# Optimization experiments

Measured on AMD Instinct MI355X. Metric: run time of the kernel, lower is better.

## Reference

```python
import jax, jax.numpy as jnp
import numpy as np

N_ENTITY = 30000
N_REL = 12
N_BASES = 8
KG_DIM = 128
TOK_DIM = 768
B = 32
N_CTX_ENT = 50
SEQ = 256
N_EDGES = 400000
VOCAB = 30522
PAD_IDX = 0


def setup_inputs() -> dict:
    key = jax.random.key(0)
    ks = jax.random.split(key, 24)
    s = 0.02
    inp = {
        "context_entities": jax.random.randint(ks[0], (B, N_CTX_ENT), 0, N_ENTITY),
        "context_tokens": jax.random.randint(ks[1], (B, SEQ), 0, VOCAB),
        "edge_index": jax.random.randint(ks[2], (2, N_EDGES), 0, N_ENTITY),
        "edge_type": jax.random.randint(ks[3], (N_EDGES,), 0, N_REL),
        # stand-in for bert_model(...).last_hidden_state
        "token_embedding": jax.random.normal(ks[4], (B, SEQ, TOK_DIM), dtype=jnp.float32),
        # RGCN basis-decomposition params (x=None -> node-identity features)
        "comp": jax.random.normal(ks[5], (N_REL, N_BASES), dtype=jnp.float32) * s,
        "basis": jax.random.normal(ks[6], (N_BASES, N_ENTITY, KG_DIM), dtype=jnp.float32) * s,
        "root": jax.random.normal(ks[7], (N_ENTITY, KG_DIM), dtype=jnp.float32) * s,
        "rgcn_bias": jnp.zeros((KG_DIM,), dtype=jnp.float32),
        # SelfDotAttention over entity reps (dim=da=KG_DIM)
        "ent_W": jax.random.normal(ks[8], (KG_DIM, KG_DIM), dtype=jnp.float32) * s,
        "ent_b": jnp.zeros((KG_DIM,), dtype=jnp.float32),
        "ent_v": jax.random.normal(ks[9], (KG_DIM,), dtype=jnp.float32) * s,
        # AdditiveAttention over token reps (dim=da=TOK_DIM)
        "tok_W": jax.random.normal(ks[10], (TOK_DIM, TOK_DIM), dtype=jnp.float32) * s,
        "tok_b": jnp.zeros((TOK_DIM,), dtype=jnp.float32),
        "tok_v": jax.random.normal(ks[11], (TOK_DIM,), dtype=jnp.float32) * s,
        # linear_transformation: token_emb_dim -> kg_emb_dim
        "lin_W": jax.random.normal(ks[12], (KG_DIM, TOK_DIM), dtype=jnp.float32) * s,
        "lin_b": jnp.zeros((KG_DIM,), dtype=jnp.float32),
        # gating: 2*kg_emb_dim -> kg_emb_dim
        "gate_W": jax.random.normal(ks[13], (KG_DIM, 2 * KG_DIM), dtype=jnp.float32) * s,
        "gate_b": jnp.zeros((KG_DIM,), dtype=jnp.float32),
    }
    return inp


def _rgcn(comp, basis, root, bias, edge_index, edge_type):
    # composed per-relation weight over identity features: [R, N, D]
    weight = jnp.einsum('rb,bnd->rnd', comp, basis)
    src, dst = edge_index[0], edge_index[1]
    msg = weight[edge_type, src]                      # [E, D] gather
    # per-relation, per-target mean aggregation (PyG RGCNConv aggr='mean')
    seg = edge_type * N_ENTITY + dst
    cnt = jax.ops.segment_sum(jnp.ones((msg.shape[0],), msg.dtype), seg,
                              num_segments=N_REL * N_ENTITY)
    norm = 1.0 / jnp.maximum(cnt[seg], 1.0)
    agg = jax.ops.segment_sum(msg * norm[:, None], dst, num_segments=N_ENTITY)
    return agg + root + bias                          # [N, D]


def _attn_pool(h, mask, W, b, v):
    # e = v^T tanh(h W + b); masked softmax; weighted sum over sequence
    e = jnp.einsum('bld,d->bl', jnp.tanh(jnp.einsum('bld,de->ble', h, W) + b), v)
    e = jnp.where(mask, e, jnp.asarray(-1e9, h.dtype))
    a = jax.nn.softmax(e, axis=-1)
    return jnp.einsum('bl,bld->bd', a, h)


def reference(context_entities, context_tokens, edge_index, edge_type,
              token_embedding, comp, basis, root, rgcn_bias,
              ent_W, ent_b, ent_v, tok_W, tok_b, tok_v,
              lin_W, lin_b, gate_W, gate_b):
    kg_embedding = _rgcn(comp, basis, root, rgcn_bias, edge_index, edge_type)

    entity_reps = kg_embedding[context_entities]              # [B, L_e, D]
    entity_mask = context_entities != PAD_IDX
    entity_attn_rep = _attn_pool(entity_reps, entity_mask, ent_W, ent_b, ent_v)

    token_mask = context_tokens != PAD_IDX
    token_attn_rep = _attn_pool(token_embedding, token_mask, tok_W, tok_b, tok_v)
    token_attn_rep = token_attn_rep @ lin_W.T + lin_b         # [B, D]

    gate = jax.nn.sigmoid(
        jnp.concatenate([token_attn_rep, entity_attn_rep], axis=1) @ gate_W.T + gate_b)
    user_embedding = gate * token_attn_rep + (1.0 - gate) * entity_attn_rep

    scores = user_embedding @ kg_embedding.T                  # [B, N_ENTITY]
    return scores
```

## Files before the change

### kernel.cpp

```cpp
#include <hip/hip_runtime.h>
#include <hip/hip_bf16.h>
#include <math.h>

#define N_ENTITY 30000
#define N_REL    12
#define N_BASES  8
#define KG_DIM   128
#define TOK_DIM  768
#define BATCH    32
#define N_CTX    50
#define SEQ      256
#define N_EDGES  400000

#define W8_SCALE 1024.0f
#define W8_INV   (1.0f / 1024.0f)

#define OFF_KG     0
#define OFF_CNT    3840000
#define OFF_DEG    4200000
#define OFF_START  4230000
#define OFF_CURSOR 4260004
#define OFF_CHUNK  4290004
#define OFF_SR     4290068
#define OFF_ETOK   5090068
#define OFF_ENT    5098260
#define OFF_TOK    5102356
#define OFF_USER   5106452
#define OFF_W      5110548
#define OFF_ABF    5110548
#define OFF_WBF    8256276
#define NEED_W_BYTES ((size_t)(OFF_W + 11520000) * 4)

typedef __bf16 bf16x8 __attribute__((ext_vector_type(8)));
typedef float  floatx4 __attribute__((ext_vector_type(4)));

__device__ __forceinline__ float tanh_fast(float x) {
    float ax = fabsf(x);
    float e = __expf(-2.0f * ax);
    float t = 1.0f - 2.0f * e / (1.0f + e);
    return copysignf(t, x);
}

__global__ void zero_kernel(int* __restrict__ p, int n) {
    int i = blockIdx.x * 256 + threadIdx.x;
    if (i < n) p[i] = 0;
}

__global__ void count_kernel(const int* __restrict__ edge_index,
                             const int* __restrict__ edge_type,
                             int* __restrict__ cnt) {
    int e = blockIdx.x * 256 + threadIdx.x;
    if (e >= N_EDGES) return;
    int r = edge_type[e];
    int dst = edge_index[N_EDGES + e];
    atomicAdd(&cnt[r * N_ENTITY + dst], 1);
}

__global__ __launch_bounds__(1024) void scan1_kernel(const int* __restrict__ cnt,
                                                     int* __restrict__ deg,
                                                     int* __restrict__ start,
                                                     int* __restrict__ chunksum) {
    __shared__ int wsum[16];
    int tid = threadIdx.x, lane = tid & 63, wv = tid >> 6;
    int i = blockIdx.x * 1024 + tid;
    int v = 0;
    if (i < N_ENTITY) {
#pragma unroll
        for (int r = 0; r < N_REL; ++r) v += cnt[r * N_ENTITY + i];
        deg[i] = v;
    }
    int x = v;
#pragma unroll
    for (int off = 1; off < 64; off <<= 1) {
        int t = __shfl_up(x, off);
        if (lane >= off) x += t;
    }
    if (lane == 63) wsum[wv] = x;
    __syncthreads();
    if (wv == 0 && lane < 16) {
        int w = wsum[lane];
#pragma unroll
        for (int off = 1; off < 16; off <<= 1) {
            int t = __shfl_up(w, off);
            if (lane >= off) w += t;
        }
        wsum[lane] = w;
    }
    __syncthreads();
    int wbase = (wv == 0) ? 0 : wsum[wv - 1];
    if (i < N_ENTITY) start[i] = wbase + x - v;
    if (tid == 1023) chunksum[blockIdx.x] = wbase + x;
}

__global__ __launch_bounds__(256) void scan2_kernel(const int* __restrict__ chunksum,
                                                    int* __restrict__ chunkoff,
                                                    int* __restrict__ start,
                                                    int* __restrict__ zp) {
    int tid = threadIdx.x;
    if (tid < 64) {
        int lane = tid;
        int v = (lane < 30) ? chunksum[lane] : 0;
        int x = v;
#pragma unroll
        for (int off = 1; off < 64; off <<= 1) {
            int t = __shfl_up(x, off);
            if (lane >= off) x += t;
        }
        if (lane < 30) chunkoff[lane] = x - v;
        if (lane == 63) start[N_ENTITY] = x;
    }
    for (int i = tid; i < 20480; i += 256) zp[i] = 0;
}

__global__ __launch_bounds__(1024) void scan3_kernel(const int* __restrict__ chunkoff,
                                                     int* __restrict__ start,
                                                     int* __restrict__ cursor) {
    int i = blockIdx.x * 1024 + threadIdx.x;
    if (i < N_ENTITY) {
        int s = start[i] + chunkoff[blockIdx.x];
        start[i] = s;
        cursor[i] = s;
    }
}

__global__ void place_kernel(const int* __restrict__ edge_index,
                             const int* __restrict__ edge_type,
                             const int* __restrict__ cnt,
                             int* __restrict__ cursor,
                             int2* __restrict__ er) {
    int e = blockIdx.x * 256 + threadIdx.x;
    if (e >= N_EDGES) return;
    int r = edge_type[e];
    int src = edge_index[e];
    int dst = edge_index[N_EDGES + e];
    int c = cnt[r * N_ENTITY + dst];
    float norm = 1.0f / (float)(c > 1 ? c : 1);
    int slot = atomicAdd(&cursor[dst], 1);
    er[slot] = make_int2(src | (r << 15), __float_as_int(norm));
}

__global__ void weight_fp8_kernel(const float* __restrict__ comp,
                                  const float4* __restrict__ basis4,
                                  unsigned int* __restrict__ w1) {
    int idx = blockIdx.x * 256 + threadIdx.x;
    float4 bv[N_BASES];
#pragma unroll
    for (int i = 0; i < N_BASES; ++i) bv[i] = basis4[(size_t)i * 960000 + idx];
#pragma unroll
    for (int r = 0; r < N_REL; ++r) {
        float s0 = 0.f, s1 = 0.f, s2 = 0.f, s3 = 0.f;
#pragma unroll
        for (int i = 0; i < N_BASES; ++i) {
            float c = comp[r * N_BASES + i];
            s0 += c * bv[i].x; s1 += c * bv[i].y;
            s2 += c * bv[i].z; s3 += c * bv[i].w;
        }
        int pk = __builtin_amdgcn_cvt_pk_fp8_f32(s0 * W8_SCALE, s1 * W8_SCALE, 0, false);
        pk = __builtin_amdgcn_cvt_pk_fp8_f32(s2 * W8_SCALE, s3 * W8_SCALE, pk, true);
        w1[(size_t)r * 960000 + idx] = (unsigned int)pk;
    }
}

__global__ __launch_bounds__(256) void gather_kernel(const int* __restrict__ start,
                                                     const int* __restrict__ deg,
                                                     const int2* __restrict__ er,
                                                     const unsigned short* __restrict__ w8,
                                                     const float2* __restrict__ root2,
                                                     const float2* __restrict__ bias2,
                                                     float2* __restrict__ kg2) {
    int wv = threadIdx.x >> 6, lane = threadIdx.x & 63;
    int dst = blockIdx.x * 4 + wv;
    if (dst >= N_ENTITY) return;
    int s = start[dst], n = deg[dst];
    float ax = 0.f, ay = 0.f;
    int j = 0;
    for (; j + 1 < n; j += 2) {
        int2 e0 = er[s + j], e1 = er[s + j + 1];
        float n0 = __int_as_float(e0.y), n1 = __int_as_float(e1.y);
        int s0 = e0.x & 32767, r0 = e0.x >> 15;
        int s1 = e1.x & 32767, r1 = e1.x >> 15;
        int u0 = (int)w8[((size_t)(r0 * N_ENTITY + s0) << 6) + lane];
        int u1 = (int)w8[((size_t)(r1 * N_ENTITY + s1) << 6) + lane];
        ax += __builtin_amdgcn_cvt_f32_fp8(u0, 0) * n0 +
              __builtin_amdgcn_cvt_f32_fp8(u1, 0) * n1;
        ay += __builtin_amdgcn_cvt_f32_fp8(u0, 1) * n0 +
              __builtin_amdgcn_cvt_f32_fp8(u1, 1) * n1;
    }
    if (j < n) {
        int2 e0 = er[s + j];
        float n0 = __int_as_float(e0.y);
        int s0 = e0.x & 32767, r0 = e0.x >> 15;
        int u0 = (int)w8[((size_t)(r0 * N_ENTITY + s0) << 6) + lane];
        ax += __builtin_amdgcn_cvt_f32_fp8(u0, 0) * n0;
        ay += __builtin_amdgcn_cvt_f32_fp8(u0, 1) * n0;
    }
    float2 rt = root2[(size_t)dst * 64 + lane];
    float2 bs = bias2[lane];
    kg2[(size_t)dst * 64 + lane] = make_float2(ax * W8_INV + rt.x + bs.x,
                                               ay * W8_INV + rt.y + bs.y);
}

__global__ __launch_bounds__(256) void gather_otf_kernel(const int* __restrict__ start,
                                                         const int* __restrict__ deg,
                                                         const int2* __restrict__ er,
                                                         const float* __restrict__ comp,
                                                         const float2* __restrict__ basis2,
                                                         const float2* __restrict__ root2,
                                                         const float2* __restrict__ bias2,
                                                         float2* __restrict__ kg2) {
    int wv = threadIdx.x >> 6, lane = threadIdx.x & 63;
    int dst = blockIdx.x * 4 + wv;
    if (dst >= N_ENTITY) return;
    int s = start[dst], n = deg[dst];
    float ax = 0.f, ay = 0.f;
    for (int j = 0; j < n; ++j) {
        int2 e0 = er[s + j];
        float nm = __int_as_float(e0.y);
        int src = e0.x & 32767, r = e0.x >> 15;
        float mx = 0.f, my = 0.f;
#pragma unroll
        for (int b = 0; b < N_BASES; ++b) {
            float cf = comp[r * N_BASES + b];
            float2 bs = basis2[((size_t)b * N_ENTITY + src) * 64 + lane];
            mx += cf * bs.x; my += cf * bs.y;
        }
        ax += mx * nm; ay += my * nm;
    }
    float2 rt = root2[(size_t)dst * 64 + lane];
    float2 bs = bias2[lane];
    kg2[(size_t)dst * 64 + lane] = make_float2(ax + rt.x + bs.x, ay + rt.y + bs.y);
}

__global__ __launch_bounds__(256) void ent_attn_kernel(const int* __restrict__ ctx_ent,
                                                       const float* __restrict__ kg,
                                                       const float* __restrict__ W,
                                                       const float* __restrict__ bb,
                                                       const float* __restrict__ v,
                                                       float* __restrict__ ent_rep) {
    __shared__ __align__(16) float Ws[KG_DIM * KG_DIM];
    __shared__ __align__(16) float h[N_CTX * KG_DIM];
    __shared__ float es[64];
    __shared__ int ids[N_CTX];
    int b = blockIdx.x, tid = threadIdx.x;
    if (tid < N_CTX) ids[tid] = ctx_ent[b * N_CTX + tid];
    __syncthreads();
    for (int i = tid; i < N_CTX * 32; i += 256) {
        int l = i >> 5, d4 = i & 31;
        ((float4*)h)[i] = ((const float4*)kg)[(size_t)ids[l] * 32 + d4];
    }
    for (int i = tid; i < KG_DIM * KG_DIM / 4; i += 256)
        ((float4*)Ws)[i] = ((const float4*)W)[i];
    __syncthreads();

    int wave = tid >> 6, lane = tid & 63;
    const int nl = (N_CTX - wave + 3) / 4;
    float s0[13], s1[13];
#pragma unroll
    for (int i = 0; i < 13; ++i) { s0[i] = 0.f; s1[i] = 0.f; }
    for (int k4 = 0; k4 < 32; ++k4) {
        float4 hk[13];
#pragma unroll
        for (int i = 0; i < 13; ++i)
            if (i < nl) hk[i] = ((const float4*)h)[(wave + i * 4) * 32 + k4];
#pragma unroll
        for (int kk = 0; kk < 4; ++kk) {
            int k = k4 * 4 + kk;
            float w0 = Ws[k * KG_DIM + lane];
            float w1 = Ws[k * KG_DIM + lane + 64];
#pragma unroll
            for (int i = 0; i < 13; ++i) {
                if (i < nl) {
                    float hv = (&hk[i].x)[kk];
                    s0[i] += hv * w0;
                    s1[i] += hv * w1;
                }
            }
        }
    }
    float bias0 = bb[lane], bias1 = bb[lane + 64];
    float v0 = v[lane], v1 = v[lane + 64];
    for (int i = 0; i < nl; ++i) {
        int l = wave + i * 4;
        float p = tanhf(s0[i] + bias0) * v0 + tanhf(s1[i] + bias1) * v1;
        p += __shfl_xor(p, 32); p += __shfl_xor(p, 16); p += __shfl_xor(p, 8);
        p += __shfl_xor(p, 4);  p += __shfl_xor(p, 2);  p += __shfl_xor(p, 1);
        if (lane == 0) es[l] = p;
    }
    __syncthreads();
    if (tid < 64) {
        float val = (tid < N_CTX && ids[tid] != 0) ? es[tid] : -1e9f;
        float mx = val;
        mx = fmaxf(mx, __shfl_xor(mx, 32)); mx = fmaxf(mx, __shfl_xor(mx, 16));
        mx = fmaxf(mx, __shfl_xor(mx, 8));  mx = fmaxf(mx, __shfl_xor(mx, 4));
        mx = fmaxf(mx, __shfl_xor(mx, 2));  mx = fmaxf(mx, __shfl_xor(mx, 1));
        float ex = (tid < N_CTX) ? expf(val - mx) : 0.f;
        float sm = ex;
        sm += __shfl_xor(sm, 32); sm += __shfl_xor(sm, 16); sm += __shfl_xor(sm, 8);
        sm += __shfl_xor(sm, 4);  sm += __shfl_xor(sm, 2);  sm += __shfl_xor(sm, 1);
        if (tid < N_CTX) es[tid] = ex / sm;
    }
    __syncthreads();
    if (tid < KG_DIM) {
        float o = 0.f;
#pragma unroll
        for (int l = 0; l < N_CTX; ++l) o += es[l] * h[l * KG_DIM + tid];
        ent_rep[b * KG_DIM + tid] = o;
    }
}


__global__ void convA_kernel(const float* __restrict__ in, __bf16* __restrict__ out,
                             int n8) {
    int i = blockIdx.x * 256 + threadIdx.x;
    if (i >= n8) return;
    const float4* p = (const float4*)(in + (size_t)i * 8);
    float4 a = p[0], b = p[1];
    union { __bf16 h[8]; uint4 u; } r;
    r.h[0] = (__bf16)a.x; r.h[1] = (__bf16)a.y; r.h[2] = (__bf16)a.z; r.h[3] = (__bf16)a.w;
    r.h[4] = (__bf16)b.x; r.h[5] = (__bf16)b.y; r.h[6] = (__bf16)b.z; r.h[7] = (__bf16)b.w;
    *(uint4*)(out + (size_t)i * 8) = r.u;
}

__global__ void convWT_kernel(const float* __restrict__ W, __bf16* __restrict__ Wt) {
    __shared__ float tile[64][65];
    int tx = threadIdx.x & 63, ty = threadIdx.x >> 6;
    int kb = blockIdx.x * 64, cb = blockIdx.y * 64;
#pragma unroll
    for (int i = 0; i < 16; ++i) {
        int r = ty + i * 4;
        tile[r][tx] = W[(size_t)(kb + r) * TOK_DIM + cb + tx];
    }
    __syncthreads();
#pragma unroll
    for (int i = 0; i < 16; ++i) {
        int r = ty + i * 4;
        Wt[(size_t)(cb + r) * TOK_DIM + kb + tx] = (__bf16)tile[tx][r];
    }
}

__global__ __launch_bounds__(256) void tok_gemm_kernel(const __bf16* __restrict__ A,
                                                       const __bf16* __restrict__ Bt,
                                                       const float* __restrict__ bias,
                                                       const float* __restrict__ v,
                                                       float* __restrict__ e_out) {
    __shared__ __align__(16) __bf16 sA[4096];
    __shared__ __align__(16) __bf16 sB[4096];
    int tid = threadIdx.x;
    int wave = tid >> 6, lane = tid & 63;
    int wm = wave >> 1, wn = wave & 1;
    int quad = lane >> 4, idx = lane & 15;
    int m0 = blockIdx.y * 128, c0 = blockIdx.x * 128;

    int rowS = tid & 127, kpS = tid >> 7;
    const __bf16* gA0 = A + (size_t)(m0 + rowS) * TOK_DIM + kpS * 8;
    const __bf16* gA1 = gA0 + 16;
    const __bf16* gB0 = Bt + (size_t)(c0 + rowS) * TOK_DIM + kpS * 8;
    const __bf16* gB1 = gB0 + 16;
    __bf16* dA0 = &sA[tid * 8];
    __bf16* dA1 = &sA[tid * 8 + 2048];
    __bf16* dB0 = &sB[tid * 8];
    __bf16* dB1 = &sB[tid * 8 + 2048];

    floatx4 acc[4][4];
#pragma unroll
    for (int mi = 0; mi < 4; ++mi)
#pragma unroll
        for (int ni = 0; ni < 4; ++ni)
            acc[mi][ni] = (floatx4){0.f, 0.f, 0.f, 0.f};

    for (int k0 = 0; k0 < TOK_DIM; k0 += 32) {
        uint4 ra0 = *(const uint4*)(gA0 + k0);
        uint4 ra1 = *(const uint4*)(gA1 + k0);
        uint4 rb0 = *(const uint4*)(gB0 + k0);
        uint4 rb1 = *(const uint4*)(gB1 + k0);
        __syncthreads();
        *(uint4*)dA0 = ra0; *(uint4*)dA1 = ra1;
        *(uint4*)dB0 = rb0; *(uint4*)dB1 = rb1;
        __syncthreads();
        bf16x8 aF[4], bF[4];
#pragma unroll
        for (int i = 0; i < 4; ++i) {
            aF[i] = *(const bf16x8*)&sA[quad * 1024 + (wm * 64 + i * 16 + idx) * 8];
            bF[i] = *(const bf16x8*)&sB[quad * 1024 + (wn * 64 + i * 16 + idx) * 8];
        }
#pragma unroll
        for (int mi = 0; mi < 4; ++mi)
#pragma unroll
            for (int ni = 0; ni < 4; ++ni)
                acc[mi][ni] = __builtin_amdgcn_mfma_f32_16x16x32_bf16(
                    aF[mi], bF[ni], acc[mi][ni], 0, 0, 0);
    }

    float bv[4], vv[4];
#pragma unroll
    for (int ni = 0; ni < 4; ++ni) {
        int c = c0 + wn * 64 + ni * 16 + idx;
        bv[ni] = bias[c]; vv[ni] = v[c];
    }
#pragma unroll
    for (int mi = 0; mi < 4; ++mi) {
        float s[4] = {0.f, 0.f, 0.f, 0.f};
#pragma unroll
        for (int ni = 0; ni < 4; ++ni)
#pragma unroll
            for (int r = 0; r < 4; ++r)
                s[r] += tanh_fast(acc[mi][ni][r] + bv[ni]) * vv[ni];
#pragma unroll
        for (int r = 0; r < 4; ++r) {
            s[r] += __shfl_xor(s[r], 1); s[r] += __shfl_xor(s[r], 2);
            s[r] += __shfl_xor(s[r], 4); s[r] += __shfl_xor(s[r], 8);
        }
        if (idx == 0) {
            int rbase = m0 + wm * 64 + mi * 16 + quad * 4;
#pragma unroll
            for (int r = 0; r < 4; ++r) atomicAdd(&e_out[rbase + r], s[r]);
        }
    }
}

__global__ __launch_bounds__(256) void tok_pool2_kernel(const int* __restrict__ ctx_tok,
                                                        const float* __restrict__ e_ws,
                                                        const __bf16* __restrict__ Abf,
                                                        const float* __restrict__ lin_W,
                                                        float* __restrict__ tok_rep) {
    __shared__ float a_s[SEQ];
    __shared__ float4 part[8][32];
    __shared__ __align__(16) float pooled[128];
    __shared__ float redm[4];
    __shared__ float reds[4];
    int b = blockIdx.x, c = blockIdx.y;
    int tid = threadIdx.x;
    int wave = tid >> 6, lane = tid & 63;
    int t = ctx_tok[b * SEQ + tid];
    float val = (t != 0) ? e_ws[b * SEQ + tid] : -1e9f;
    float mx = val;
    mx = fmaxf(mx, __shfl_xor(mx, 32)); mx = fmaxf(mx, __shfl_xor(mx, 16));
    mx = fmaxf(mx, __shfl_xor(mx, 8));  mx = fmaxf(mx, __shfl_xor(mx, 4));
    mx = fmaxf(mx, __shfl_xor(mx, 2));  mx = fmaxf(mx, __shfl_xor(mx, 1));
    if (lane == 0) redm[wave] = mx;
    __syncthreads();
    mx = fmaxf(fmaxf(redm[0], redm[1]), fmaxf(redm[2], redm[3]));
    float ex = expf(val - mx);
    float sm = ex;
    sm += __shfl_xor(sm, 32); sm += __shfl_xor(sm, 16); sm += __shfl_xor(sm, 8);
    sm += __shfl_xor(sm, 4);  sm += __shfl_xor(sm, 2);  sm += __shfl_xor(sm, 1);
    if (lane == 0) reds[wave] = sm;
    __syncthreads();
    sm = reds[0] + reds[1] + reds[2] + reds[3];
    a_s[tid] = ex / sm;
    __syncthreads();
    int d4 = tid & 31, lg = tid >> 5;
    const unsigned int* eb = (const unsigned int*)(Abf + (size_t)b * SEQ * TOK_DIM +
                                                   c * 128 + d4 * 4);
    float4 acc = make_float4(0.f, 0.f, 0.f, 0.f);
    for (int l = lg; l < SEQ; l += 8) {
        float al = a_s[l];
        unsigned int u0 = eb[(size_t)l * 384];
        unsigned int u1 = eb[(size_t)l * 384 + 1];
        acc.x += al * __uint_as_float(u0 << 16);
        acc.y += al * __uint_as_float(u0 & 0xffff0000u);
        acc.z += al * __uint_as_float(u1 << 16);
        acc.w += al * __uint_as_float(u1 & 0xffff0000u);
    }
    part[lg][d4] = acc;
    __syncthreads();
    if (tid < 32) {
        float4 s = part[0][tid];
#pragma unroll
        for (int g = 1; g < 8; ++g) {
            float4 p = part[g][tid];
            s.x += p.x; s.y += p.y; s.z += p.z; s.w += p.w;
        }
        ((float4*)pooled)[tid] = s;
    }
    __syncthreads();
    int d = tid & 127, hf = tid >> 7;
    const float* wr = lin_W + (size_t)d * TOK_DIM + c * 128 + hf * 64;
    float s = 0.f;
#pragma unroll 8
    for (int k = 0; k < 64; ++k) s += pooled[hf * 64 + k] * wr[k];
    atomicAdd(&tok_rep[b * KG_DIM + d], s);
}

__global__ void gate_kernel(const float* __restrict__ tok_rep,
                            const float* __restrict__ lin_b,
                            const float* __restrict__ ent_rep,
                            const float* __restrict__ gate_W,
                            const float* __restrict__ gate_b,
                            float* __restrict__ user) {
    __shared__ float tr[KG_DIM], er[KG_DIM];
    int b = blockIdx.x, d = threadIdx.x;
    tr[d] = tok_rep[b * KG_DIM + d] + lin_b[d];
    er[d] = ent_rep[b * KG_DIM + d];
    __syncthreads();
    float g = gate_b[d];
    const float* wr = gate_W + (size_t)d * 256;
#pragma unroll 8
    for (int k = 0; k < KG_DIM; ++k) g += tr[k] * wr[k] + er[k] * wr[KG_DIM + k];
    float sig = 1.f / (1.f + expf(-g));
    user[b * KG_DIM + d] = sig * tr[d] + (1.f - sig) * er[d];
}

__global__ void scores_kernel(const float* __restrict__ user,
                              const float4* __restrict__ kg4,
                              float* __restrict__ out) {
    __shared__ float4 u4[BATCH * 32];
    int tid = threadIdx.x;
    for (int i = tid; i < BATCH * 32; i += 256) u4[i] = ((const float4*)user)[i];
    __syncthreads();
    int n = blockIdx.x * 256 + tid;
    if (n >= N_ENTITY) return;
    float acc[BATCH];
#pragma unroll
    for (int b = 0; b < BATCH; ++b) acc[b] = 0.f;
    for (int d4 = 0; d4 < 32; ++d4) {
        float4 k = kg4[(size_t)n * 32 + d4];
#pragma unroll
        for (int b = 0; b < BATCH; ++b) {
            float4 u = u4[b * 32 + d4];
            acc[b] += k.x * u.x + k.y * u.y + k.z * u.z + k.w * u.w;
        }
    }
    for (int b = 0; b < BATCH; ++b) out[(size_t)b * N_ENTITY + n] = acc[b];
}

extern "C" void kernel_launch(void* const* d_in, const int* in_sizes, int n_in,
                              void* d_out, int out_size, void* d_ws, size_t ws_size,
                              hipStream_t stream) {
    (void)in_sizes; (void)n_in; (void)out_size;
    const int*   ctx_ent   = (const int*)d_in[0];
    const int*   ctx_tok   = (const int*)d_in[1];
    const int*   edge_index= (const int*)d_in[2];
    const int*   edge_type = (const int*)d_in[3];
    const float* tok_emb   = (const float*)d_in[4];
    const float* comp      = (const float*)d_in[5];
    const float* basis     = (const float*)d_in[6];
    const float* root      = (const float*)d_in[7];
    const float* rgcn_bias = (const float*)d_in[8];
    const float* ent_W     = (const float*)d_in[9];
    const float* ent_b     = (const float*)d_in[10];
    const float* ent_v     = (const float*)d_in[11];
    const float* tok_W     = (const float*)d_in[12];
    const float* tok_b     = (const float*)d_in[13];
    const float* tok_v     = (const float*)d_in[14];
    const float* lin_W     = (const float*)d_in[15];
    const float* lin_b     = (const float*)d_in[16];
    const float* gate_W    = (const float*)d_in[17];
    const float* gate_b    = (const float*)d_in[18];
    float* scores = (float*)d_out;

    float* ws = (float*)d_ws;
    float* kg      = ws + OFF_KG;
    int*   cnt     = (int*)(ws + OFF_CNT);
    int*   deg     = (int*)(ws + OFF_DEG);
    int*   start   = (int*)(ws + OFF_START);
    int*   cursor  = (int*)(ws + OFF_CURSOR);
    int*   chunk   = (int*)(ws + OFF_CHUNK);
    int2*  er      = (int2*)(ws + OFF_SR);
    float* e_ws    = ws + OFF_ETOK;
    float* ent_rep = ws + OFF_ENT;
    float* tok_rep = ws + OFF_TOK;
    float* user    = ws + OFF_USER;
    float* weight  = ws + OFF_W;
    __bf16* Abf    = (__bf16*)(ws + OFF_ABF);
    __bf16* Wbf    = (__bf16*)(ws + OFF_WBF);
    const bool use_weight = (ws_size >= NEED_W_BYTES);

    zero_kernel<<<(360000 + 255) / 256, 256, 0, stream>>>(cnt, 360000);
    count_kernel<<<(N_EDGES + 255) / 256, 256, 0, stream>>>(edge_index, edge_type, cnt);
    scan1_kernel<<<30, 1024, 0, stream>>>(cnt, deg, start, chunk);
    scan2_kernel<<<1, 256, 0, stream>>>(chunk, chunk + 32, start, (int*)e_ws);
    scan3_kernel<<<30, 1024, 0, stream>>>(chunk + 32, start, cursor);
    place_kernel<<<(N_EDGES + 255) / 256, 256, 0, stream>>>(edge_index, edge_type, cnt,
                                                            cursor, er);
    if (use_weight) {
        weight_fp8_kernel<<<3750, 256, 0, stream>>>(comp, (const float4*)basis,
                                                    (unsigned int*)weight);
        gather_kernel<<<(N_ENTITY + 3) / 4, 256, 0, stream>>>(
            start, deg, er, (const unsigned short*)weight, (const float2*)root,
            (const float2*)rgcn_bias, (float2*)kg);
    } else {
        gather_otf_kernel<<<(N_ENTITY + 3) / 4, 256, 0, stream>>>(
            start, deg, er, comp, (const float2*)basis, (const float2*)root,
            (const float2*)rgcn_bias, (float2*)kg);
    }
    ent_attn_kernel<<<BATCH, 256, 0, stream>>>(ctx_ent, kg, ent_W, ent_b, ent_v, ent_rep);

    convA_kernel<<<(BATCH * SEQ * TOK_DIM / 8 + 255) / 256, 256, 0, stream>>>(
        tok_emb, Abf, BATCH * SEQ * TOK_DIM / 8);
    {
        dim3 g(12, 12);
        convWT_kernel<<<g, 256, 0, stream>>>(tok_W, Wbf);
    }
    {
        dim3 g(TOK_DIM / 128, BATCH * SEQ / 128);
        tok_gemm_kernel<<<g, 256, 0, stream>>>(Abf, Wbf, tok_b, tok_v, e_ws);
    }
    {
        dim3 g(BATCH, 6);
        tok_pool2_kernel<<<g, 256, 0, stream>>>(ctx_tok, e_ws, Abf, lin_W, tok_rep);
    }
    gate_kernel<<<BATCH, 128, 0, stream>>>(tok_rep, lin_b, ent_rep, gate_W, gate_b, user);
    scores_kernel<<<(N_ENTITY + 255) / 256, 256, 0, stream>>>(user, (const float4*)kg, scores);
}
```

Baseline: 470.2 us.

## Fuse independent kernels into combined launches to cut launch count and overlap work

```diff
diff --git a/kernel.cpp b/kernel.cpp
--- a/kernel.cpp
+++ b/kernel.cpp
@@ -15,21 +15,29 @@
 #define W8_SCALE 1024.0f
 #define W8_INV   (1.0f / 1024.0f)
 
+#define NCHUNK 118
+
 #define OFF_KG     0
 #define OFF_CNT    3840000
 #define OFF_DEG    4200000
 #define OFF_START  4230000
-#define OFF_CURSOR 4260004
-#define OFF_CHUNK  4290004
-#define OFF_SR     4290068
-#define OFF_ETOK   5090068
-#define OFF_ENT    5098260
-#define OFF_TOK    5102356
-#define OFF_USER   5106452
-#define OFF_W      5110548
-#define OFF_ABF    5110548
-#define OFF_WBF    8256276
-#define NEED_W_BYTES ((size_t)(OFF_W + 11520000) * 4)
+#define OFF_PC     4260000
+#define OFF_CHK    4290000
+#define OFF_SR     4290256
+#define OFF_ETOK   5090256
+#define OFF_ENT    5098448
+#define OFF_TOK    5102544
+#define OFF_USER   5106640
+#define OFF_W      5110736
+#define OFF_ABF_B  16630736
+#define OFF_WBF_B  19776464
+#define END_BIG    20071376
+#define NEED_BIG_BYTES ((size_t)END_BIG * 4)
+#define OFF_ABF_S  5110736
+#define OFF_WBF_S  8256464
+
+#define NZERO_INT  410736
+#define NZB        1605
 
 typedef __bf16 bf16x8 __attribute__((ext_vector_type(8)));
 typedef float  floatx4 __attribute__((ext_vector_type(4)));
@@ -41,93 +49,283 @@
     return copysignf(t, x);
 }
 
-__global__ void zero_kernel(int* __restrict__ p, int n) {
-    int i = blockIdx.x * 256 + threadIdx.x;
-    if (i < n) p[i] = 0;
-}
-
-__global__ void count_kernel(const int* __restrict__ edge_index,
-                             const int* __restrict__ edge_type,
-                             int* __restrict__ cnt) {
-    int e = blockIdx.x * 256 + threadIdx.x;
-    if (e >= N_EDGES) return;
-    int r = edge_type[e];
-    int dst = edge_index[N_EDGES + e];
-    atomicAdd(&cnt[r * N_ENTITY + dst], 1);
-}
-
-__global__ __launch_bounds__(1024) void scan1_kernel(const int* __restrict__ cnt,
-                                                     int* __restrict__ deg,
-                                                     int* __restrict__ start,
-                                                     int* __restrict__ chunksum) {
-    __shared__ int wsum[16];
-    int tid = threadIdx.x, lane = tid & 63, wv = tid >> 6;
-    int i = blockIdx.x * 1024 + tid;
-    int v = 0;
-    if (i < N_ENTITY) {
-#pragma unroll
-        for (int r = 0; r < N_REL; ++r) v += cnt[r * N_ENTITY + i];
-        deg[i] = v;
-    }
-    int x = v;
-#pragma unroll
-    for (int off = 1; off < 64; off <<= 1) {
-        int t = __shfl_up(x, off);
-        if (lane >= off) x += t;
-    }
-    if (lane == 63) wsum[wv] = x;
-    __syncthreads();
-    if (wv == 0 && lane < 16) {
-        int w = wsum[lane];
-#pragma unroll
-        for (int off = 1; off < 16; off <<= 1) {
-            int t = __shfl_up(w, off);
-            if (lane >= off) w += t;
-        }
-        wsum[lane] = w;
-    }
-    __syncthreads();
-    int wbase = (wv == 0) ? 0 : wsum[wv - 1];
-    if (i < N_ENTITY) start[i] = wbase + x - v;
-    if (tid == 1023) chunksum[blockIdx.x] = wbase + x;
-}
-
-__global__ __launch_bounds__(256) void scan2_kernel(const int* __restrict__ chunksum,
-                                                    int* __restrict__ chunkoff,
-                                                    int* __restrict__ start,
-                                                    int* __restrict__ zp) {
-    int tid = threadIdx.x;
-    if (tid < 64) {
-        int lane = tid;
-        int v = (lane < 30) ? chunksum[lane] : 0;
-        int x = v;
+__global__ __launch_bounds__(256) void init_fused_kernel(
+    const float* __restrict__ comp, const float4* __restrict__ basis4,
+    unsigned int* __restrict__ w1,
+    const float* __restrict__ tok_emb, __bf16* __restrict__ Abf,
+    const float* __restrict__ tok_W, __bf16* __restrict__ Wbf,
+    int* __restrict__ cnt, int* __restrict__ pc, int* __restrict__ chk,
+    int* __restrict__ accum, int wB) {
+    __shared__ float tile[64][65];
+    int bid = blockIdx.x, tid = threadIdx.x;
+    if (bid < wB) {
+        int idx = bid * 256 + tid;
+        float4 bv[N_BASES];
+#pragma unroll
+        for (int i = 0; i < N_BASES; ++i) bv[i] = basis4[(size_t)i * 960000 + idx];
+#pragma unroll
+        for (int r = 0; r < N_REL; ++r) {
+            float s0 = 0.f, s1 = 0.f, s2 = 0.f, s3 = 0.f;
+#pragma unroll
+            for (int i = 0; i < N_BASES; ++i) {
+                float c = comp[r * N_BASES + i];
+                s0 += c * bv[i].x; s1 += c * bv[i].y;
+                s2 += c * bv[i].z; s3 += c * bv[i].w;
+            }
+            int pk = __builtin_amdgcn_cvt_pk_fp8_f32(s0 * W8_SCALE, s1 * W8_SCALE, 0, false);
+            pk = __builtin_amdgcn_cvt_pk_fp8_f32(s2 * W8_SCALE, s3 * W8_SCALE, pk, true);
+            w1[(size_t)r * 960000 + idx] = (unsigned int)pk;
+        }
+        return;
+    }
+    bid -= wB;
+    if (bid < 3072) {
+        int i = bid * 256 + tid;
+        const float4* p = (const float4*)(tok_emb + (size_t)i * 8);
+        float4 a = p[0], b = p[1];
+        union { __bf16 h[8]; uint4 u; } r;
+        r.h[0] = (__bf16)a.x; r.h[1] = (__bf16)a.y; r.h[2] = (__bf16)a.z; r.h[3] = (__bf16)a.w;
+        r.h[4] = (__bf16)b.x; r.h[5] = (__bf16)b.y; r.h[6] = (__bf16)b.z; r.h[7] = (__bf16)b.w;
+        *(uint4*)(Abf + (size_t)i * 8) = r.u;
+        return;
+    }
+    bid -= 3072;
+    if (bid < NZB) {
+        int idx = bid * 256 + tid;
+        if (idx < 360000) { cnt[idx] = 0; return; }
+        idx -= 360000;
+        if (idx < 30000) { pc[idx] = 0; return; }
+        idx -= 30000;
+        if (idx < 256) { chk[idx] = 0; return; }
+        idx -= 256;
+        if (idx < 20480) accum[idx] = 0;
+        return;
+    }
+    bid -= NZB;
+    int tx = tid & 63, ty = tid >> 6;
+    int kb = (bid % 12) * 64, cb = (bid / 12) * 64;
+#pragma unroll
+    for (int i = 0; i < 16; ++i) {
+        int rr = ty + i * 4;
+        tile[rr][tx] = tok_W[(size_t)(kb + rr) * TOK_DIM + cb + tx];
+    }
+    __syncthreads();
+#pragma unroll
+    for (int i = 0; i < 16; ++i) {
+        int rr = ty + i * 4;
+        Wbf[(size_t)(cb + rr) * TOK_DIM + kb + tx] = (__bf16)tile[tx][rr];
+    }
+}
+
+__global__ __launch_bounds__(256) void count_gemm_kernel(
+    const int* __restrict__ edge_index, const int* __restrict__ edge_type,
+    int* __restrict__ cnt,
+    const __bf16* __restrict__ A, const __bf16* __restrict__ Bt,
+    const float* __restrict__ bias, const float* __restrict__ v,
+    float* __restrict__ e_out) {
+    __shared__ __align__(16) __bf16 sA[4096];
+    __shared__ __align__(16) __bf16 sB[4096];
+    int bid = blockIdx.x, tid = threadIdx.x;
+    if (bid >= 384) {
+        int e = (bid - 384) * 256 + tid;
+        if (e < N_EDGES) {
+            int r = edge_type[e];
+            int dst = edge_index[N_EDGES + e];
+            atomicAdd(&cnt[r * N_ENTITY + dst], 1);
+        }
+        return;
+    }
+    int wave = tid >> 6, lane = tid & 63;
+    int wm = wave >> 1, wn = wave & 1;
+    int quad = lane >> 4, idx = lane & 15;
+    int m0 = (bid / 6) * 128, c0 = (bid % 6) * 128;
+
+    int rowS = tid & 127, kpS = tid >> 7;
+    const __bf16* gA0 = A + (size_t)(m0 + rowS) * TOK_DIM + kpS * 8;
+    const __bf16* gA1 = gA0 + 16;
+    const __bf16* gB0 = Bt + (size_t)(c0 + rowS) * TOK_DIM + kpS * 8;
+    const __bf16* gB1 = gB0 + 16;
+    __bf16* dA0 = &sA[tid * 8];
+    __bf16* dA1 = &sA[tid * 8 + 2048];
+    __bf16* dB0 = &sB[tid * 8];
+    __bf16* dB1 = &sB[tid * 8 + 2048];
+
+    floatx4 acc[4][4];
+#pragma unroll
+    for (int mi = 0; mi < 4; ++mi)
+#pragma unroll
+        for (int ni = 0; ni < 4; ++ni)
+            acc[mi][ni] = (floatx4){0.f, 0.f, 0.f, 0.f};
+
+    for (int k0 = 0; k0 < TOK_DIM; k0 += 32) {
+        uint4 ra0 = *(const uint4*)(gA0 + k0);
+        uint4 ra1 = *(const uint4*)(gA1 + k0);
+        uint4 rb0 = *(const uint4*)(gB0 + k0);
+        uint4 rb1 = *(const uint4*)(gB1 + k0);
+        __syncthreads();
+        *(uint4*)dA0 = ra0; *(uint4*)dA1 = ra1;
+        *(uint4*)dB0 = rb0; *(uint4*)dB1 = rb1;
+        __syncthreads();
+        bf16x8 aF[4], bF[4];
+#pragma unroll
+        for (int i = 0; i < 4; ++i) {
+            aF[i] = *(const bf16x8*)&sA[quad * 1024 + (wm * 64 + i * 16 + idx) * 8];
+            bF[i] = *(const bf16x8*)&sB[quad * 1024 + (wn * 64 + i * 16 + idx) * 8];
+        }
+#pragma unroll
+        for (int mi = 0; mi < 4; ++mi)
+#pragma unroll
+            for (int ni = 0; ni < 4; ++ni)
+                acc[mi][ni] = __builtin_amdgcn_mfma_f32_16x16x32_bf16(
+                    aF[mi], bF[ni], acc[mi][ni], 0, 0, 0);
+    }
+
+    float bv[4], vv[4];
+#pragma unroll
+    for (int ni = 0; ni < 4; ++ni) {
+        int c = c0 + wn * 64 + ni * 16 + idx;
+        bv[ni] = bias[c]; vv[ni] = v[c];
+    }
+#pragma unroll
+    for (int mi = 0; mi < 4; ++mi) {
+        float s[4] = {0.f, 0.f, 0.f, 0.f};
+#pragma unroll
+        for (int ni = 0; ni < 4; ++ni)
+#pragma unroll
+            for (int r = 0; r < 4; ++r)
+                s[r] += tanh_fast(acc[mi][ni][r] + bv[ni]) * vv[ni];
+#pragma unroll
+        for (int r = 0; r < 4; ++r) {
+            s[r] += __shfl_xor(s[r], 1); s[r] += __shfl_xor(s[r], 2);
+            s[r] += __shfl_xor(s[r], 4); s[r] += __shfl_xor(s[r], 8);
+        }
+        if (idx == 0) {
+            int rbase = m0 + wm * 64 + mi * 16 + quad * 4;
+#pragma unroll
+            for (int r = 0; r < 4; ++r) atomicAdd(&e_out[rbase + r], s[r]);
+        }
+    }
+}
+
+__global__ __launch_bounds__(256) void scan_pool_kernel(
+    const int* __restrict__ cnt, int* __restrict__ deg,
+    int* __restrict__ startL, int* __restrict__ chk,
+    const int* __restrict__ ctx_tok, const float* __restrict__ e_ws,
+    const __bf16* __restrict__ Abf, const float* __restrict__ lin_W,
+    float* __restrict__ tok_rep) {
+    __shared__ int wsum[5];
+    __shared__ int lastf;
+    __shared__ int cs[NCHUNK];
+    __shared__ float a_s[SEQ];
+    __shared__ float4 part[8][32];
+    __shared__ __align__(16) float pooled[128];
+    __shared__ float redm[4];
+    __shared__ float reds[4];
+    int bid = blockIdx.x, tid = threadIdx.x;
+    if (bid < NCHUNK) {
+        int lane = tid & 63, wv = tid >> 6;
+        int i = bid * 256 + tid;
+        int val = 0;
+        if (i < N_ENTITY) {
+#pragma unroll
+            for (int r = 0; r < N_REL; ++r) val += cnt[r * N_ENTITY + i];
+            deg[i] = val;
+        }
+        int x = val;
 #pragma unroll
         for (int off = 1; off < 64; off <<= 1) {
             int t = __shfl_up(x, off);
             if (lane >= off) x += t;
         }
-        if (lane < 30) chunkoff[lane] = x - v;
-        if (lane == 63) start[N_ENTITY] = x;
-    }
-    for (int i = tid; i < 20480; i += 256) zp[i] = 0;
-}
-
-__global__ __launch_bounds__(1024) void scan3_kernel(const int* __restrict__ chunkoff,
-                                                     int* __restrict__ start,
-                                                     int* __restrict__ cursor) {
-    int i = blockIdx.x * 1024 + threadIdx.x;
-    if (i < N_ENTITY) {
-        int s = start[i] + chunkoff[blockIdx.x];
-        start[i] = s;
-        cursor[i] = s;
-    }
-}
-
-__global__ void place_kernel(const int* __restrict__ edge_index,
-                             const int* __restrict__ edge_type,
-                             const int* __restrict__ cnt,
-                             int* __restrict__ cursor,
-                             int2* __restrict__ er) {
+        if (lane == 63) wsum[wv] = x;
+        __syncthreads();
+        if (tid == 0) {
+            int a = 0;
+#pragma unroll
+            for (int w = 0; w < 4; ++w) { int t = wsum[w]; wsum[w] = a; a += t; }
+            wsum[4] = a;
+        }
+        __syncthreads();
+        if (i < N_ENTITY) startL[i] = wsum[wv] + x - val;
+        if (tid == 0) {
+            chk[bid] = wsum[4];
+            __threadfence();
+            lastf = (atomicAdd(&chk[255], 1) == NCHUNK - 1);
+        }
+        __syncthreads();
+        if (lastf) {
+            if (tid < NCHUNK) cs[tid] = atomicAdd(&chk[tid], 0);
+            __syncthreads();
+            if (tid == 0) {
+                int a = 0;
+                for (int j = 0; j < NCHUNK; ++j) { int t = cs[j]; cs[j] = a; a += t; }
+            }
+            __syncthreads();
+            if (tid < NCHUNK) chk[128 + tid] = cs[tid];
+        }
+        return;
+    }
+    int id2 = bid - NCHUNK;
+    int b = id2 & 31, c = id2 >> 5;
+    int wave = tid >> 6, lane = tid & 63;
+    int t = ctx_tok[b * SEQ + tid];
+    float val = (t != 0) ? e_ws[b * SEQ + tid] : -1e9f;
+    float mx = val;
+    mx = fmaxf(mx, __shfl_xor(mx, 32)); mx = fmaxf(mx, __shfl_xor(mx, 16));
+    mx = fmaxf(mx, __shfl_xor(mx, 8));  mx = fmaxf(mx, __shfl_xor(mx, 4));
+    mx = fmaxf(mx, __shfl_xor(mx, 2));  mx = fmaxf(mx, __shfl_xor(mx, 1));
+    if (lane == 0) redm[wave] = mx;
+    __syncthreads();
+    mx = fmaxf(fmaxf(redm[0], redm[1]), fmaxf(redm[2], redm[3]));
+    float ex = expf(val - mx);
+    float sm = ex;
+    sm += __shfl_xor(sm, 32); sm += __shfl_xor(sm, 16); sm += __shfl_xor(sm, 8);
+    sm += __shfl_xor(sm, 4);  sm += __shfl_xor(sm, 2);  sm += __shfl_xor(sm, 1);
+    if (lane == 0) reds[wave] = sm;
+    __syncthreads();
+    sm = reds[0] + reds[1] + reds[2] + reds[3];
+    a_s[tid] = ex / sm;
+    __syncthreads();
+    int d4 = tid & 31, lg = tid >> 5;
+    const unsigned int* eb = (const unsigned int*)(Abf + (size_t)b * SEQ * TOK_DIM +
+                                                   c * 128 + d4 * 4);
+    float4 acc = make_float4(0.f, 0.f, 0.f, 0.f);
+    for (int l = lg; l < SEQ; l += 8) {
+        float al = a_s[l];
+        unsigned int u0 = eb[(size_t)l * 384];
+        unsigned int u1 = eb[(size_t)l * 384 + 1];
+        acc.x += al * __uint_as_float(u0 << 16);
+        acc.y += al * __uint_as_float(u0 & 0xffff0000u);
+        acc.z += al * __uint_as_float(u1 << 16);
+        acc.w += al * __uint_as_float(u1 & 0xffff0000u);
+    }
+    part[lg][d4] = acc;
+    __syncthreads();
+    if (tid < 32) {
+        float4 s = part[0][tid];
+#pragma unroll
+        for (int g = 1; g < 8; ++g) {
+            float4 p = part[g][tid];
+            s.x += p.x; s.y += p.y; s.z += p.z; s.w += p.w;
+        }
+        ((float4*)pooled)[tid] = s;
+    }
+    __syncthreads();
+    int d = tid & 127, hf = tid >> 7;
+    const float* wr = lin_W + (size_t)d * TOK_DIM + c * 128 + hf * 64;
+    float s = 0.f;
+#pragma unroll 8
+    for (int k = 0; k < 64; ++k) s += pooled[hf * 64 + k] * wr[k];
+    atomicAdd(&tok_rep[b * KG_DIM + d], s);
+}
+
+__global__ void place2_kernel(const int* __restrict__ edge_index,
+                              const int* __restrict__ edge_type,
+                              const int* __restrict__ cnt,
+                              const int* __restrict__ startL,
+                              const int* __restrict__ chkoff,
+                              int* __restrict__ pc,
+                              int2* __restrict__ er) {
     int e = blockIdx.x * 256 + threadIdx.x;
     if (e >= N_EDGES) return;
     int r = edge_type[e];
@@ -135,43 +333,22 @@
     int dst = edge_index[N_EDGES + e];
     int c = cnt[r * N_ENTITY + dst];
     float norm = 1.0f / (float)(c > 1 ? c : 1);
-    int slot = atomicAdd(&cursor[dst], 1);
+    int slot = startL[dst] + chkoff[dst >> 8] + atomicAdd(&pc[dst], 1);
     er[slot] = make_int2(src | (r << 15), __float_as_int(norm));
 }
 
-__global__ void weight_fp8_kernel(const float* __restrict__ comp,
-                                  const float4* __restrict__ basis4,
-                                  unsigned int* __restrict__ w1) {
-    int idx = blockIdx.x * 256 + threadIdx.x;
-    float4 bv[N_BASES];
-#pragma unroll
-    for (int i = 0; i < N_BASES; ++i) bv[i] = basis4[(size_t)i * 960000 + idx];
-#pragma unroll
-    for (int r = 0; r < N_REL; ++r) {
-        float s0 = 0.f, s1 = 0.f, s2 = 0.f, s3 = 0.f;
-#pragma unroll
-        for (int i = 0; i < N_BASES; ++i) {
-            float c = comp[r * N_BASES + i];
-            s0 += c * bv[i].x; s1 += c * bv[i].y;
-            s2 += c * bv[i].z; s3 += c * bv[i].w;
-        }
-        int pk = __builtin_amdgcn_cvt_pk_fp8_f32(s0 * W8_SCALE, s1 * W8_SCALE, 0, false);
-        pk = __builtin_amdgcn_cvt_pk_fp8_f32(s2 * W8_SCALE, s3 * W8_SCALE, pk, true);
-        w1[(size_t)r * 960000 + idx] = (unsigned int)pk;
-    }
-}
-
-__global__ __launch_bounds__(256) void gather_kernel(const int* __restrict__ start,
-                                                     const int* __restrict__ deg,
-                                                     const int2* __restrict__ er,
-                                                     const unsigned short* __restrict__ w8,
-                                                     const float2* __restrict__ root2,
-                                                     const float2* __restrict__ bias2,
-                                                     float2* __restrict__ kg2) {
+__global__ __launch_bounds__(256) void gather2_kernel(const int* __restrict__ startL,
+                                                      const int* __restrict__ chkoff,
+                                                      const int* __restrict__ deg,
+                                                      const int2* __restrict__ er,
+                                                      const unsigned short* __restrict__ w8,
+                                                      const float2* __restrict__ root2,
+                                                      const float2* __restrict__ bias2,
+                                                      float2* __restrict__ kg2) {
     int wv = threadIdx.x >> 6, lane = threadIdx.x & 63;
     int dst = blockIdx.x * 4 + wv;
     if (dst >= N_ENTITY) return;
-    int s = start[dst], n = deg[dst];
+    int s = startL[dst] + chkoff[dst >> 8], n = deg[dst];
     float ax = 0.f, ay = 0.f;
     int j = 0;
     for (; j + 1 < n; j += 2) {
@@ -200,18 +377,19 @@
                                                ay * W8_INV + rt.y + bs.y);
 }
 
-__global__ __launch_bounds__(256) void gather_otf_kernel(const int* __restrict__ start,
-                                                         const int* __restrict__ deg,
-                                                         const int2* __restrict__ er,
-                                                         const float* __restrict__ comp,
-                                                         const float2* __restrict__ basis2,
-                                                         const float2* __restrict__ root2,
-                                                         const float2* __restrict__ bias2,
-                                                         float2* __restrict__ kg2) {
+__global__ __launch_bounds__(256) void gather2_otf_kernel(const int* __restrict__ startL,
+                                                          const int* __restrict__ chkoff,
+                                                          const int* __restrict__ deg,
+                                                          const int2* __restrict__ er,
+                                                          const float* __restrict__ comp,
+                                                          const float2* __restrict__ basis2,
+                                                          const float2* __restrict__ root2,
+                                                          const float2* __restrict__ bias2,
+                                                          float2* __restrict__ kg2) {
     int wv = threadIdx.x >> 6, lane = threadIdx.x & 63;
     int dst = blockIdx.x * 4 + wv;
     if (dst >= N_ENTITY) return;
-    int s = start[dst], n = deg[dst];
+    int s = startL[dst] + chkoff[dst >> 8], n = deg[dst];
     float ax = 0.f, ay = 0.f;
     for (int j = 0; j < n; ++j) {
         int2 e0 = er[s + j];
@@ -231,16 +409,18 @@
     kg2[(size_t)dst * 64 + lane] = make_float2(ax + rt.x + bs.x, ay + rt.y + bs.y);
 }
 
-__global__ __launch_bounds__(256) void ent_attn_kernel(const int* __restrict__ ctx_ent,
-                                                       const float* __restrict__ kg,
-                                                       const float* __restrict__ W,
-                                                       const float* __restrict__ bb,
-                                                       const float* __restrict__ v,
-                                                       float* __restrict__ ent_rep) {
+__global__ __launch_bounds__(256) void ent_attn_gate_kernel(
+    const int* __restrict__ ctx_ent, const float* __restrict__ kg,
+    const float* __restrict__ W, const float* __restrict__ bb,
+    const float* __restrict__ v, const float* __restrict__ tok_rep,
+    const float* __restrict__ lin_b, const float* __restrict__ gate_W,
+    const float* __restrict__ gate_b, float* __restrict__ user) {
     __shared__ __align__(16) float Ws[KG_DIM * KG_DIM];
     __shared__ __align__(16) float h[N_CTX * KG_DIM];
     __shared__ float es[64];
     __shared__ int ids[N_CTX];
+    __shared__ float ers[KG_DIM];
+    __shared__ float trs[KG_DIM];
     int b = blockIdx.x, tid = threadIdx.x;
     if (tid < N_CTX) ids[tid] = ctx_ent[b * N_CTX + tid];
     __syncthreads();
@@ -304,201 +484,18 @@
         float o = 0.f;
 #pragma unroll
         for (int l = 0; l < N_CTX; ++l) o += es[l] * h[l * KG_DIM + tid];
-        ent_rep[b * KG_DIM + tid] = o;
-    }
-}
-
-
-__global__ void convA_kernel(const float* __restrict__ in, __bf16* __restrict__ out,
-                             int n8) {
-    int i = blockIdx.x * 256 + threadIdx.x;
-    if (i >= n8) return;
-    const float4* p = (const float4*)(in + (size_t)i * 8);
-    float4 a = p[0], b = p[1];
-    union { __bf16 h[8]; uint4 u; } r;
-    r.h[0] = (__bf16)a.x; r.h[1] = (__bf16)a.y; r.h[2] = (__bf16)a.z; r.h[3] = (__bf16)a.w;
-    r.h[4] = (__bf16)b.x; r.h[5] = (__bf16)b.y; r.h[6] = (__bf16)b.z; r.h[7] = (__bf16)b.w;
-    *(uint4*)(out + (size_t)i * 8) = r.u;
-}
-
-__global__ void convWT_kernel(const float* __restrict__ W, __bf16* __restrict__ Wt) {
-    __shared__ float tile[64][65];
-    int tx = threadIdx.x & 63, ty = threadIdx.x >> 6;
-    int kb = blockIdx.x * 64, cb = blockIdx.y * 64;
-#pragma unroll
-    for (int i = 0; i < 16; ++i) {
-        int r = ty + i * 4;
-        tile[r][tx] = W[(size_t)(kb + r) * TOK_DIM + cb + tx];
-    }
-    __syncthreads();
-#pragma unroll
-    for (int i = 0; i < 16; ++i) {
-        int r = ty + i * 4;
-        Wt[(size_t)(cb + r) * TOK_DIM + kb + tx] = (__bf16)tile[tx][r];
-    }
-}
-
-__global__ __launch_bounds__(256) void tok_gemm_kernel(const __bf16* __restrict__ A,
-                                                       const __bf16* __restrict__ Bt,
-                                                       const float* __restrict__ bias,
-                                                       const float* __restrict__ v,
-                                                       float* __restrict__ e_out) {
-    __shared__ __align__(16) __bf16 sA[4096];
-    __shared__ __align__(16) __bf16 sB[4096];
-    int tid = threadIdx.x;
-    int wave = tid >> 6, lane = tid & 63;
-    int wm = wave >> 1, wn = wave & 1;
-    int quad = lane >> 4, idx = lane & 15;
-    int m0 = blockIdx.y * 128, c0 = blockIdx.x * 128;
-
-    int rowS = tid & 127, kpS = tid >> 7;
-    const __bf16* gA0 = A + (size_t)(m0 + rowS) * TOK_DIM + kpS * 8;
-    const __bf16* gA1 = gA0 + 16;
-    const __bf16* gB0 = Bt + (size_t)(c0 + rowS) * TOK_DIM + kpS * 8;
-    const __bf16* gB1 = gB0 + 16;
-    __bf16* dA0 = &sA[tid * 8];
-    __bf16* dA1 = &sA[tid * 8 + 2048];
-    __bf16* dB0 = &sB[tid * 8];
-    __bf16* dB1 = &sB[tid * 8 + 2048];
-
-    floatx4 acc[4][4];
-#pragma unroll
-    for (int mi = 0; mi < 4; ++mi)
-#pragma unroll
-        for (int ni = 0; ni < 4; ++ni)
-            acc[mi][ni] = (floatx4){0.f, 0.f, 0.f, 0.f};
-
-    for (int k0 = 0; k0 < TOK_DIM; k0 += 32) {
-        uint4 ra0 = *(const uint4*)(gA0 + k0);
-        uint4 ra1 = *(const uint4*)(gA1 + k0);
-        uint4 rb0 = *(const uint4*)(gB0 + k0);
-        uint4 rb1 = *(const uint4*)(gB1 + k0);
-        __syncthreads();
-        *(uint4*)dA0 = ra0; *(uint4*)dA1 = ra1;
-        *(uint4*)dB0 = rb0; *(uint4*)dB1 = rb1;
-        __syncthreads();
-        bf16x8 aF[4], bF[4];
-#pragma unroll
-        for (int i = 0; i < 4; ++i) {
-            aF[i] = *(const bf16x8*)&sA[quad * 1024 + (wm * 64 + i * 16 + idx) * 8];
-            bF[i] = *(const bf16x8*)&sB[quad * 1024 + (wn * 64 + i * 16 + idx) * 8];
-        }
-#pragma unroll
-        for (int mi = 0; mi < 4; ++mi)
-#pragma unroll
-            for (int ni = 0; ni < 4; ++ni)
-                acc[mi][ni] = __builtin_amdgcn_mfma_f32_16x16x32_bf16(
-                    aF[mi], bF[ni], acc[mi][ni], 0, 0, 0);
-    }
-
-    float bv[4], vv[4];
-#pragma unroll
-    for (int ni = 0; ni < 4; ++ni) {
-        int c = c0 + wn * 64 + ni * 16 + idx;
-        bv[ni] = bias[c]; vv[ni] = v[c];
-    }
-#pragma unroll
-    for (int mi = 0; mi < 4; ++mi) {
-        float s[4] = {0.f, 0.f, 0.f, 0.f};
-#pragma unroll
-        for (int ni = 0; ni < 4; ++ni)
-#pragma unroll
-            for (int r = 0; r < 4; ++r)
-                s[r] += tanh_fast(acc[mi][ni][r] + bv[ni]) * vv[ni];
-#pragma unroll
-        for (int r = 0; r < 4; ++r) {
-            s[r] += __shfl_xor(s[r], 1); s[r] += __shfl_xor(s[r], 2);
-            s[r] += __shfl_xor(s[r], 4); s[r] += __shfl_xor(s[r], 8);
-        }
-        if (idx == 0) {
-            int rbase = m0 + wm * 64 + mi * 16 + quad * 4;
-#pragma unroll
-            for (int r = 0; r < 4; ++r) atomicAdd(&e_out[rbase + r], s[r]);
-        }
-    }
-}
-
-__global__ __launch_bounds__(256) void tok_pool2_kernel(const int* __restrict__ ctx_tok,
-                                                        const float* __restrict__ e_ws,
-                                                        const __bf16* __restrict__ Abf,
-                                                        const float* __restrict__ lin_W,
-                                                        float* __restrict__ tok_rep) {
-    __shared__ float a_s[SEQ];
-    __shared__ float4 part[8][32];
-    __shared__ __align__(16) float pooled[128];
-    __shared__ float redm[4];
-    __shared__ float reds[4];
-    int b = blockIdx.x, c = blockIdx.y;
-    int tid = threadIdx.x;
-    int wave = tid >> 6, lane = tid & 63;
-    int t = ctx_tok[b * SEQ + tid];
-    float val = (t != 0) ? e_ws[b * SEQ + tid] : -1e9f;
-    float mx = val;
-    mx = fmaxf(mx, __shfl_xor(mx, 32)); mx = fmaxf(mx, __shfl_xor(mx, 16));
-    mx = fmaxf(mx, __shfl_xor(mx, 8));  mx = fmaxf(mx, __shfl_xor(mx, 4));
-    mx = fmaxf(mx, __shfl_xor(mx, 2));  mx = fmaxf(mx, __shfl_xor(mx, 1));
-    if (lane == 0) redm[wave] = mx;
-    __syncthreads();
-    mx = fmaxf(fmaxf(redm[0], redm[1]), fmaxf(redm[2], redm[3]));
-    float ex = expf(val - mx);
-    float sm = ex;
-    sm += __shfl_xor(sm, 32); sm += __shfl_xor(sm, 16); sm += __shfl_xor(sm, 8);
-    sm += __shfl_xor(sm, 4);  sm += __shfl_xor(sm, 2);  sm += __shfl_xor(sm, 1);
-    if (lane == 0) reds[wave] = sm;
-    __syncthreads();
-    sm = reds[0] + reds[1] + reds[2] + reds[3];
-    a_s[tid] = ex / sm;
-    __syncthreads();
-    int d4 = tid & 31, lg = tid >> 5;
-    const unsigned int* eb = (const unsigned int*)(Abf + (size_t)b * SEQ * TOK_DIM +
-                                                   c * 128 + d4 * 4);
-    float4 acc = make_float4(0.f, 0.f, 0.f, 0.f);
-    for (int l = lg; l < SEQ; l += 8) {
-        float al = a_s[l];
-        unsigned int u0 = eb[(size_t)l * 384];
-        unsigned int u1 = eb[(size_t)l * 384 + 1];
-        acc.x += al * __uint_as_float(u0 << 16);
-        acc.y += al * __uint_as_float(u0 & 0xffff0000u);
-        acc.z += al * __uint_as_float(u1 << 16);
-        acc.w += al * __uint_as_float(u1 & 0xffff0000u);
-    }
-    part[lg][d4] = acc;
-    __syncthreads();
-    if (tid < 32) {
-        float4 s = part[0][tid];
-#pragma unroll
-        for (int g = 1; g < 8; ++g) {
-            float4 p = part[g][tid];
-            s.x += p.x; s.y += p.y; s.z += p.z; s.w += p.w;
-        }
-        ((float4*)pooled)[tid] = s;
-    }
-    __syncthreads();
-    int d = tid & 127, hf = tid >> 7;
-    const float* wr = lin_W + (size_t)d * TOK_DIM + c * 128 + hf * 64;
-    float s = 0.f;
+        ers[tid] = o;
+        trs[tid] = tok_rep[b * KG_DIM + tid] + lin_b[tid];
+    }
+    __syncthreads();
+    if (tid < KG_DIM) {
+        float g = gate_b[tid];
+        const float* wr = gate_W + (size_t)tid * 256;
 #pragma unroll 8
-    for (int k = 0; k < 64; ++k) s += pooled[hf * 64 + k] * wr[k];
-    atomicAdd(&tok_rep[b * KG_DIM + d], s);
-}
-
-__global__ void gate_kernel(const float* __restrict__ tok_rep,
-                            const float* __restrict__ lin_b,
-                            const float* __restrict__ ent_rep,
-                            const float* __restrict__ gate_W,
-                            const float* __restrict__ gate_b,
-                            float* __restrict__ user) {
-    __shared__ float tr[KG_DIM], er[KG_DIM];
-    int b = blockIdx.x, d = threadIdx.x;
-    tr[d] = tok_rep[b * KG_DIM + d] + lin_b[d];
-    er[d] = ent_rep[b * KG_DIM + d];
-    __syncthreads();
-    float g = gate_b[d];
-    const float* wr = gate_W + (size_t)d * 256;
-#pragma unroll 8
-    for (int k = 0; k < KG_DIM; ++k) g += tr[k] * wr[k] + er[k] * wr[KG_DIM + k];
-    float sig = 1.f / (1.f + expf(-g));
-    user[b * KG_DIM + d] = sig * tr[d] + (1.f - sig) * er[d];
+        for (int k = 0; k < KG_DIM; ++k) g += trs[k] * wr[k] + ers[k] * wr[KG_DIM + k];
+        float sig = 1.f / (1.f + expf(-g));
+        user[b * KG_DIM + tid] = sig * trs[tid] + (1.f - sig) * ers[tid];
+    }
 }
 
 __global__ void scores_kernel(const float* __restrict__ user,
@@ -553,53 +550,39 @@
     float* kg      = ws + OFF_KG;
     int*   cnt     = (int*)(ws + OFF_CNT);
     int*   deg     = (int*)(ws + OFF_DEG);
-    int*   start   = (int*)(ws + OFF_START);
-    int*   cursor  = (int*)(ws + OFF_CURSOR);
-    int*   chunk   = (int*)(ws + OFF_CHUNK);
+    int*   startL  = (int*)(ws + OFF_START);
+    int*   pc      = (int*)(ws + OFF_PC);
+    int*   chk     = (int*)(ws + OFF_CHK);
     int2*  er      = (int2*)(ws + OFF_SR);
     float* e_ws    = ws + OFF_ETOK;
-    float* ent_rep = ws + OFF_ENT;
     float* tok_rep = ws + OFF_TOK;
     float* user    = ws + OFF_USER;
     float* weight  = ws + OFF_W;
-    __bf16* Abf    = (__bf16*)(ws + OFF_ABF);
-    __bf16* Wbf    = (__bf16*)(ws + OFF_WBF);
-    const bool use_weight = (ws_size >= NEED_W_BYTES);
-
-    zero_kernel<<<(360000 + 255) / 256, 256, 0, stream>>>(cnt, 360000);
-    count_kernel<<<(N_EDGES + 255) / 256, 256, 0, stream>>>(edge_index, edge_type, cnt);
-    scan1_kernel<<<30, 1024, 0, stream>>>(cnt, deg, start, chunk);
-    scan2_kernel<<<1, 256, 0, stream>>>(chunk, chunk + 32, start, (int*)e_ws);
-    scan3_kernel<<<30, 1024, 0, stream>>>(chunk + 32, start, cursor);
-    place_kernel<<<(N_EDGES + 255) / 256, 256, 0, stream>>>(edge_index, edge_type, cnt,
-                                                            cursor, er);
-    if (use_weight) {
-        weight_fp8_kernel<<<3750, 256, 0, stream>>>(comp, (const float4*)basis,
-                                                    (unsigned int*)weight);
-        gather_kernel<<<(N_ENTITY + 3) / 4, 256, 0, stream>>>(
-            start, deg, er, (const unsigned short*)weight, (const float2*)root,
-            (const float2*)rgcn_bias, (float2*)kg);
-    } else {
-        gather_otf_kernel<<<(N_ENTITY + 3) / 4, 256, 0, stream>>>(
-            start, deg, er, comp, (const float2*)basis, (const float2*)root,
-            (const float2*)rgcn_bias, (float2*)kg);
-    }
-    ent_attn_kernel<<<BATCH, 256, 0, stream>>>(ctx_ent, kg, ent_W, ent_b, ent_v, ent_rep);
-
-    convA_kernel<<<(BATCH * SEQ * TOK_DIM / 8 + 255) / 256, 256, 0, stream>>>(
-        tok_emb, Abf, BATCH * SEQ * TOK_DIM / 8);
-    {
-        dim3 g(12, 12);
-        convWT_kernel<<<g, 256, 0, stream>>>(tok_W, Wbf);
-    }
-    {
-        dim3 g(TOK_DIM / 128, BATCH * SEQ / 128);
-        tok_gemm_kernel<<<g, 256, 0, stream>>>(Abf, Wbf, tok_b, tok_v, e_ws);
-    }
-    {
-        dim3 g(BATCH, 6);
-        tok_pool2_kernel<<<g, 256, 0, stream>>>(ctx_tok, e_ws, Abf, lin_W, tok_rep);
-    }
-    gate_kernel<<<BATCH, 128, 0, stream>>>(tok_rep, lin_b, ent_rep, gate_W, gate_b, user);
-    scores_kernel<<<(N_ENTITY + 255) / 256, 256, 0, stream>>>(user, (const float4*)kg, scores);
-}
+
+    const bool big = (ws_size >= NEED_BIG_BYTES);
+    __bf16* Abf = (__bf16*)(ws + (big ? OFF_ABF_B : OFF_ABF_S));
+    __bf16* Wbf = (__bf16*)(ws + (big ? OFF_WBF_B : OFF_WBF_S));
+    const int wB = big ? 3750 : 0;
+
+    init_fused_kernel<<<wB + 3072 + NZB + 144, 256, 0, stream>>>(
+        comp, (const float4*)basis, (unsigned int*)weight, tok_emb, Abf, tok_W, Wbf,
+        cnt, pc, chk, (int*)e_ws, wB);
+    count_gemm_kernel<<<384 + (N_EDGES + 255) / 256, 256, 0, stream>>>(
+        edge_index, edge_type, cnt, Abf, Wbf, tok_b, tok_v, e_ws);
+    scan_pool_kernel<<<NCHUNK + 192, 256, 0, stream>>>(
+        cnt, deg, startL, chk, ctx_tok, e_ws, Abf, lin_W, tok_rep);
+    place2_kernel<<<(N_EDGES + 255) / 256, 256, 0, stream>>>(
+        edge_index, edge_type, cnt, startL, chk + 128, pc, er);
+    if (big)
+        gather2_kernel<<<(N_ENTITY + 3) / 4, 256, 0, stream>>>(
+            startL, chk + 128, deg, er, (const unsigned short*)weight,
+            (const float2*)root, (const float2*)rgcn_bias, (float2*)kg);
+    else
+        gather2_otf_kernel<<<(N_ENTITY + 3) / 4, 256, 0, stream>>>(
+            startL, chk + 128, deg, er, comp, (const float2*)basis,
+            (const float2*)root, (const float2*)rgcn_bias, (float2*)kg);
+    ent_attn_gate_kernel<<<BATCH, 256, 0, stream>>>(
+        ctx_ent, kg, ent_W, ent_b, ent_v, tok_rep, lin_b, gate_W, gate_b, user);
+    scores_kernel<<<(N_ENTITY + 255) / 256, 256, 0, stream>>>(
+        user, (const float4*)kg, scores);
+}
```

Measured after the change: 434.6 us. 7.6% less time.
